# Kernel tuning notes

Measured on AMD Instinct MI355X. Metric: run time of the kernel, lower is better.

Reference implementation:

```python
import jax, jax.numpy as jnp
import numpy as np

N_NODES = 50000
N_EDGES = 800000
N_GRAPHS = 256
IN_CH = 128
HID = 256
FFN = 256
OUT = 1


def xavier(key, shape):
    fan_in, fan_out = shape[0], shape[1]
    a = jnp.sqrt(6.0 / (fan_in + fan_out))
    return jax.random.uniform(key, shape, jnp.float32, -a, a)


def setup_inputs() -> dict:
    key = jax.random.key(0)
    ks = jax.random.split(key, 12)
    x = jax.random.normal(ks[0], (N_NODES, IN_CH), jnp.float32)
    edge_index = jax.random.randint(ks[1], (2, N_EDGES), 0, N_NODES, jnp.int32)
    batch = jnp.sort(jax.random.randint(ks[2], (N_NODES,), 0, N_GRAPHS, jnp.int32))
    return {
        "x": x,
        "edge_index": edge_index,
        "batch": batch,
        # GCNConv layers (glorot weight, zero bias as in PyG reset_parameters)
        "W1": xavier(ks[3], (IN_CH, HID)), "b1": jnp.zeros((HID,), jnp.float32),
        "W2": xavier(ks[4], (HID, HID)),   "b2": jnp.zeros((HID,), jnp.float32),
        "W3": xavier(ks[5], (HID, HID)),   "b3": jnp.zeros((HID,), jnp.float32),
        # FFN: Linear(HID, FFN) then final Linear(FFN, OUT)
        "Wf": xavier(ks[6], (HID, FFN)),   "bf": jnp.zeros((FFN,), jnp.float32),
        "Wo": xavier(ks[7], (FFN, OUT)),   "bo": jnp.zeros((OUT,), jnp.float32),
    }


def _gcn_norm(edge_index, n_nodes):
    # add self-loops, compute symmetric normalization D^-1/2 (A+I) D^-1/2
    loops = jnp.arange(n_nodes, dtype=edge_index.dtype)
    row = jnp.concatenate([edge_index[0], loops])
    col = jnp.concatenate([edge_index[1], loops])
    deg = jax.ops.segment_sum(jnp.ones_like(col, jnp.float32), col, num_segments=n_nodes)
    dis = jnp.where(deg > 0, jax.lax.rsqrt(jnp.maximum(deg, 1.0)), 0.0)
    norm = dis[row] * dis[col]  # [E+N]
    return row, col, norm


def _gcn_conv(x, W, b, row, col, norm, n_nodes):
    xw = x @ W                                   # [N, H]
    msg = xw[row] * norm[:, None]                # gather + scale  [E+N, H]
    out = jax.ops.segment_sum(msg, col, num_segments=n_nodes)
    return out + b


def reference(x, edge_index, batch, W1, b1, W2, b2, W3, b3, Wf, bf, Wo, bo):
    row, col, norm = _gcn_norm(edge_index, N_NODES)
    h = jax.nn.relu(_gcn_conv(x, W1, b1, row, col, norm, N_NODES))
    h = jax.nn.relu(_gcn_conv(h, W2, b2, row, col, norm, N_NODES))
    h = jax.nn.relu(_gcn_conv(h, W3, b3, row, col, norm, N_NODES))
    # global mean pool over graphs
    counts = jax.ops.segment_sum(jnp.ones((N_NODES,), jnp.float32), batch, num_segments=N_GRAPHS)
    pooled = jax.ops.segment_sum(h, batch, num_segments=N_GRAPHS) / jnp.maximum(counts, 1.0)[:, None]
    # FFN (dropout is identity in eval mode): Linear -> ReLU -> final Linear
    g = jax.nn.relu(pooled @ Wf + bf)
    out = g @ Wo + bo
    return out
```

## Files before the change

### kernel.cpp

```cpp
#include <hip/hip_runtime.h>
#include <hip/hip_bf16.h>
#include <hip/hip_fp16.h>


#define THREADS 256

typedef _Float16 f16x8 __attribute__((ext_vector_type(8)));
typedef float    f32x4 __attribute__((ext_vector_type(4)));


__global__ void degree_goff_kernel(const int* __restrict__ col, int* __restrict__ deg, int E,
                                   const int* __restrict__ batch, int* __restrict__ goff,
                                   int N, int G) {
    int i = blockIdx.x * THREADS + threadIdx.x;
    if (i < E) atomicAdd(&deg[col[i]], 1);
    if (i < N) {
        int b1 = batch[i];
        int b0 = (i == 0) ? -1 : batch[i - 1];
        for (int g = b0 + 1; g <= b1; ++g) goff[g] = i;
        if (i == N - 1) {
            for (int g = b1 + 1; g <= G; ++g) goff[g] = N;
        }
    }
}

__global__ __launch_bounds__(256) void scanA_kernel(
    const int* __restrict__ in, int* __restrict__ out, int* __restrict__ bsum,
    float* __restrict__ dis, int n) {
    __shared__ int wsum[4];
    int i0 = blockIdx.x * 1024 + threadIdx.x * 4;
    int lane = threadIdx.x & 63, wid = threadIdx.x >> 6;
    int v0 = 0, v1 = 0, v2 = 0, v3 = 0;
    if (i0 + 3 < n) {
        int4 v = *(const int4*)&in[i0];
        v0 = v.x; v1 = v.y; v2 = v.z; v3 = v.w;
    } else {
        if (i0 + 0 < n) v0 = in[i0 + 0];
        if (i0 + 1 < n) v1 = in[i0 + 1];
        if (i0 + 2 < n) v2 = in[i0 + 2];
        if (i0 + 3 < n) v3 = in[i0 + 3];
    }
    if (i0 + 0 < n) dis[i0 + 0] = rsqrtf((float)(v0 + 1));
    if (i0 + 1 < n) dis[i0 + 1] = rsqrtf((float)(v1 + 1));
    if (i0 + 2 < n) dis[i0 + 2] = rsqrtf((float)(v2 + 1));
    if (i0 + 3 < n) dis[i0 + 3] = rsqrtf((float)(v3 + 1));
    int s = v0 + v1 + v2 + v3;
    int inc = s;
    #pragma unroll
    for (int d = 1; d < 64; d <<= 1) {
        int t = __shfl_up(inc, d);
        if (lane >= d) inc += t;
    }
    if (lane == 63) wsum[wid] = inc;
    __syncthreads();
    int add = 0;
    for (int w = 0; w < wid; ++w) add += wsum[w];
    int ex = add + inc - s;
    if (i0 + 0 < n) out[i0 + 0] = ex;
    if (i0 + 1 < n) out[i0 + 1] = ex + v0;
    if (i0 + 2 < n) out[i0 + 2] = ex + v0 + v1;
    if (i0 + 3 < n) out[i0 + 3] = ex + v0 + v1 + v2;
    if (threadIdx.x == 255) bsum[blockIdx.x] = add + inc;
}

__global__ void scanB_kernel(int* __restrict__ bsum, int* __restrict__ total_slot, int nb) {
    int lane = threadIdx.x;
    int v = (lane < nb) ? bsum[lane] : 0;
    int inc = v;
    #pragma unroll
    for (int d = 1; d < 64; d <<= 1) {
        int t = __shfl_up(inc, d);
        if (lane >= d) inc += t;
    }
    if (lane < nb) bsum[lane] = inc - v;
    if (lane == 63) *total_slot = inc;
}

__global__ void csr_fill_kernel(const int* __restrict__ row, const int* __restrict__ col,
                                const int* __restrict__ offs, int* __restrict__ deg,
                                int* __restrict__ srcs, int E) {
    int e = blockIdx.x * THREADS + threadIdx.x;
    if (e < E) {
        int c = col[e];
        int old = atomicSub(&deg[c], 1);
        srcs[offs[c] + old - 1] = row[e];
    }
}

__global__ void convert_kernel(
    int* __restrict__ offs, const int* __restrict__ bsum, int Nfix,
    const float* __restrict__ X, const float* __restrict__ dis,
    _Float16* __restrict__ Xs, int total8, int IC,
    const float* __restrict__ W1, _Float16* __restrict__ W1t, int k1,
    const float* __restrict__ W2, _Float16* __restrict__ W2t,
    const float* __restrict__ W3, _Float16* __restrict__ W3t) {
    int i = blockIdx.x * THREADS + threadIdx.x;
    if (i < Nfix) {
        offs[i] += bsum[i >> 10];
        return;
    }
    int j = i - Nfix;
    if (j < total8) {
        int idx = j * 8;
        float d = dis[idx / IC];
        float4 a = *(const float4*)&X[idx];
        float4 b = *(const float4*)&X[idx + 4];
        f16x8 o;
        o[0] = (_Float16)(d * a.x); o[1] = (_Float16)(d * a.y);
        o[2] = (_Float16)(d * a.z); o[3] = (_Float16)(d * a.w);
        o[4] = (_Float16)(d * b.x); o[5] = (_Float16)(d * b.y);
        o[6] = (_Float16)(d * b.z); o[7] = (_Float16)(d * b.w);
        *(f16x8*)&Xs[idx] = o;
        return;
    }
    j -= total8;
    int n1 = k1 * 256;
    if (j < n1) {
        int k = j >> 8, n = j & 255;
        W1t[n * k1 + k] = (_Float16)W1[j];
        return;
    }
    j -= n1;
    if (j < 65536) {
        int k = j >> 8, n = j & 255;
        W2t[n * 256 + k] = (_Float16)W2[j];
        return;
    }
    j -= 65536;
    if (j < 65536) {
        int k = j >> 8, n = j & 255;
        W3t[n * 256 + k] = (_Float16)W3[j];
    }
}


template<int LPN>
__global__ __launch_bounds__(256) void aggregate_f16_kernel(
    const _Float16* __restrict__ X, const int* __restrict__ offs,
    const int* __restrict__ srcs, const float* __restrict__ dis,
    _Float16* __restrict__ A, int N) {
    constexpr int NPB = 256 / LPN;
    int node = blockIdx.x * NPB + threadIdx.x / LPN;
    if (node >= N) return;
    int lane = threadIdx.x % LPN;
    const f16x8* Xv = (const f16x8*)X;
    f16x8 self = Xv[(size_t)node * LPN + lane];
    float acc[8], acc2[8];
    #pragma unroll
    for (int j = 0; j < 8; ++j) { acc[j] = (float)self[j]; acc2[j] = 0.f; }
    int s = offs[node], e = offs[node + 1];
    int i = s;
    for (; i + 4 <= e; i += 4) {
        int s0 = srcs[i], s1 = srcs[i + 1], s2 = srcs[i + 2], s3 = srcs[i + 3];
        f16x8 v0 = Xv[(size_t)s0 * LPN + lane];
        f16x8 v1 = Xv[(size_t)s1 * LPN + lane];
        f16x8 v2 = Xv[(size_t)s2 * LPN + lane];
        f16x8 v3 = Xv[(size_t)s3 * LPN + lane];
        #pragma unroll
        for (int j = 0; j < 8; ++j) {
            acc[j]  += (float)v0[j] + (float)v2[j];
            acc2[j] += (float)v1[j] + (float)v3[j];
        }
    }
    for (; i < e; ++i) {
        int s0 = srcs[i];
        f16x8 v0 = Xv[(size_t)s0 * LPN + lane];
        #pragma unroll
        for (int j = 0; j < 8; ++j) acc[j] += (float)v0[j];
    }
    float dn = dis[node];
    f16x8 o;
    #pragma unroll
    for (int j = 0; j < 8; ++j) o[j] = (_Float16)(dn * (acc[j] + acc2[j]));
    ((f16x8*)A)[(size_t)node * LPN + lane] = o;
}


template<int K, int MODE>
__global__ __launch_bounds__(256) void gemm_f16_kernel(
    const _Float16* __restrict__ A, const _Float16* __restrict__ B,
    const float* __restrict__ bias, const float* __restrict__ dscale,
    _Float16* __restrict__ H, float* __restrict__ pooled,
    const int* __restrict__ batch, int M) {
    constexpr int BM = 128, BN = 128, LST = 40;
    __shared__ _Float16 As[BM * LST];
    __shared__ _Float16 Bs[BN * LST];
    __shared__ int bsh[BM];
    int lin = blockIdx.x;
    int y = (lin >> 4) * 8 + (lin & 7);
    int xh = (lin >> 3) & 1;
    int MT = (M + 127) >> 7;
    if (y >= MT) return;
    int tid = threadIdx.x;
    int m0 = y * BM, n0 = xh * BN;
    int wid = tid >> 6, lane = tid & 63;
    int wm = (wid & 1) * 64, wn = (wid >> 1) * 64;
    int l16 = lane & 15, quad = lane >> 4;

    if (MODE == 2) {
        if (tid < BM) bsh[tid] = batch[min(m0 + tid, M - 1)];
    }

    f32x4 acc[4][4] = {};

    #pragma unroll
    for (int k0 = 0; k0 < K; k0 += 32) {
        #pragma unroll
        for (int rep = 0; rep < 2; ++rep) {
            int idx = tid + rep * 256;
            int r = idx >> 2, seg = idx & 3;
            int gr = m0 + r;
            uint4 va = make_uint4(0, 0, 0, 0);
            if (gr < M) va = *(const uint4*)&A[(size_t)gr * K + k0 + seg * 8];
            *(uint4*)&As[r * LST + seg * 8] = va;
            uint4 vb = *(const uint4*)&B[(size_t)(n0 + r) * K + k0 + seg * 8];
            *(uint4*)&Bs[r * LST + seg * 8] = vb;
        }
        __syncthreads();
        f16x8 bh[4];
        #pragma unroll
        for (int ni = 0; ni < 4; ++ni) {
            int n = wn + ni * 16 + l16;
            bh[ni] = *(const f16x8*)&Bs[n * LST + quad * 8];
        }
        #pragma unroll
        for (int mi = 0; mi < 4; ++mi) {
            int m = wm + mi * 16 + l16;
            f16x8 ah = *(const f16x8*)&As[m * LST + quad * 8];
            #pragma unroll
            for (int ni = 0; ni < 4; ++ni) {
                acc[mi][ni] = __builtin_amdgcn_mfma_f32_16x16x32_f16(ah, bh[ni], acc[mi][ni], 0, 0, 0);
            }
        }
        __syncthreads();
    }

    #pragma unroll
    for (int mi = 0; mi < 4; ++mi) {
        int base_local = wm + mi * 16;
        int g0 = 0, g15 = 0;
        if (MODE == 2) { g0 = bsh[base_local]; g15 = bsh[base_local + 15]; }
        #pragma unroll
        for (int ni = 0; ni < 4; ++ni) {
            int col = n0 + wn + ni * 16 + l16;
            float bv = bias[col];
            if (MODE == 1) {
                #pragma unroll
                for (int r = 0; r < 4; ++r) {
                    int grow = m0 + base_local + quad * 4 + r;
                    if (grow < M) {
                        float v = fmaxf(acc[mi][ni][r] + bv, 0.f) * dscale[grow];
                        H[(size_t)grow * 256 + col] = (_Float16)v;
                    }
                }
            } else {
                if (g0 == g15) {
                    float p = 0.f;
                    #pragma unroll
                    for (int r = 0; r < 4; ++r) {
                        int grow = m0 + base_local + quad * 4 + r;
                        float v = fmaxf(acc[mi][ni][r] + bv, 0.f);
                        p += (grow < M) ? v : 0.f;
                    }
                    p += __shfl_xor(p, 16);
                    p += __shfl_xor(p, 32);
                    if (quad == 0) atomicAdd(&pooled[g0 * 256 + col], p);
                } else {
                    #pragma unroll
                    for (int r = 0; r < 4; ++r) {
                        int local = base_local + quad * 4 + r;
                        int grow = m0 + local;
                        if (grow < M) {
                            float v = fmaxf(acc[mi][ni][r] + bv, 0.f);
                            atomicAdd(&pooled[bsh[local] * 256 + col], v);
                        }
                    }
                }
            }
        }
    }
}


__global__ __launch_bounds__(256) void ffn_kernel(
    const float* __restrict__ pooled, const int* __restrict__ goff,
    const float* __restrict__ Wf, const float* __restrict__ bf,
    const float* __restrict__ Wo, const float* __restrict__ bo,
    float* __restrict__ out) {
    __shared__ float p[256];
    __shared__ float red[256];
    int g = blockIdx.x, t = threadIdx.x;
    int cnt = goff[g + 1] - goff[g];
    float inv = 1.f / (float)max(cnt, 1);
    p[t] = pooled[g * 256 + t] * inv;
    __syncthreads();
    float s = bf[t];
    #pragma unroll 8
    for (int k = 0; k < 256; ++k) s = fmaf(p[k], Wf[k * 256 + t], s);
    float gv = fmaxf(s, 0.f);
    red[t] = gv * Wo[t];
    __syncthreads();
    for (int o = 128; o > 0; o >>= 1) {
        if (t < o) red[t] += red[t + o];
        __syncthreads();
    }
    if (t == 0) out[g] = red[0] + bo[0];
}


extern "C" void kernel_launch(void* const* d_in, const int* in_sizes, int n_in,
                              void* d_out, int out_size, void* d_ws, size_t ws_size,
                              hipStream_t stream) {
    const float* x   = (const float*)d_in[0];
    const int*   ei  = (const int*)d_in[1];
    const int*   bat = (const int*)d_in[2];
    const float* W1  = (const float*)d_in[3];
    const float* b1  = (const float*)d_in[4];
    const float* W2  = (const float*)d_in[5];
    const float* b2  = (const float*)d_in[6];
    const float* W3  = (const float*)d_in[7];
    const float* b3  = (const float*)d_in[8];
    const float* Wf  = (const float*)d_in[9];
    const float* bf  = (const float*)d_in[10];
    const float* Wo  = (const float*)d_in[11];
    const float* bo  = (const float*)d_in[12];
    float* out = (float*)d_out;

    const int N  = in_sizes[2];
    const int E  = in_sizes[1] / 2;
    const int IC = in_sizes[0] / N;
    const int HID = 256;
    const int G  = out_size;
    const int* row = ei;
    const int* col = ei + E;

    char* w = (char*)d_ws;
    size_t off = 0;
    auto alloc = [&](size_t bytes) -> void* {
        void* p = w + off;
        off += (bytes + 255) & ~(size_t)255;
        return p;
    };
    int*   deg    = (int*)alloc((size_t)N * 4);
    float* pooled = (float*)alloc((size_t)G * HID * 4);
    float* dis    = (float*)alloc((size_t)N * 4);
    int*   offs   = (int*)alloc((size_t)(N + 1) * 4);
    int*   srcs   = (int*)alloc((size_t)E * 4);
    int*   goff   = (int*)alloc((size_t)(G + 1) * 4);
    int*   bsum   = (int*)alloc((size_t)64 * 4);
    _Float16* W1t = (_Float16*)alloc((size_t)HID * IC * 2);
    _Float16* W2t = (_Float16*)alloc((size_t)HID * HID * 2);
    _Float16* W3t = (_Float16*)alloc((size_t)HID * HID * 2);
    _Float16* Xs  = (_Float16*)alloc((size_t)N * IC * 2);
    _Float16* Ah  = (_Float16*)alloc((size_t)N * HID * 2);
    _Float16* Hs  = (_Float16*)alloc((size_t)N * HID * 2);
    (void)ws_size; (void)n_in;

    size_t zlen = (((size_t)N * 4 + 255) & ~(size_t)255) + (size_t)G * HID * 4;
    hipMemsetAsync(deg, 0, zlen, stream);

    int nb = (N + 1023) / 1024;
    degree_goff_kernel<<<(E + THREADS - 1) / THREADS, THREADS, 0, stream>>>(
        col, deg, E, bat, goff, N, G);
    scanA_kernel<<<nb, 256, 0, stream>>>(deg, offs, bsum, dis, N);
    scanB_kernel<<<1, 64, 0, stream>>>(bsum, &offs[N], nb);

    int total8 = N * IC / 8;
    int conv_total = N + total8 + IC * HID + HID * HID + HID * HID;
    convert_kernel<<<(conv_total + THREADS - 1) / THREADS, THREADS, 0, stream>>>(
        offs, bsum, N, x, dis, Xs, total8, IC, W1, W1t, IC, W2, W2t, W3, W3t);

    csr_fill_kernel<<<(E + THREADS - 1) / THREADS, THREADS, 0, stream>>>(row, col, offs, deg, srcs, E);

    int MT = (N + 127) / 128;
    int gblocks = 2 * (((MT + 7) / 8) * 8);
    aggregate_f16_kernel<16><<<(N + 15) / 16, 256, 0, stream>>>(Xs, offs, srcs, dis, Ah, N);
    gemm_f16_kernel<128, 1><<<gblocks, 256, 0, stream>>>(Ah, W1t, b1, dis, Hs, nullptr, nullptr, N);
    aggregate_f16_kernel<32><<<(N + 7) / 8, 256, 0, stream>>>(Hs, offs, srcs, dis, Ah, N);
    gemm_f16_kernel<256, 1><<<gblocks, 256, 0, stream>>>(Ah, W2t, b2, dis, Hs, nullptr, nullptr, N);
    aggregate_f16_kernel<32><<<(N + 7) / 8, 256, 0, stream>>>(Hs, offs, srcs, dis, Ah, N);
    gemm_f16_kernel<256, 2><<<gblocks, 256, 0, stream>>>(Ah, W3t, b3, nullptr, nullptr, pooled, bat, N);

    ffn_kernel<<<G, 256, 0, stream>>>(pooled, goff, Wf, bf, Wo, bo, out);
}
```

Baseline: 439.2 us.

## Make GEMM persistent with full weight matrix resident in shared memory

Replaces the tiled 128x128 GEMM with a persistent kernel. Each block loads the whole transposed weight matrix into LDS once, then loops over 64-row tiles. A fragments are read straight from global memory into registers and the per-k-step syncthreads are gone. This removes repeated weight staging and barrier overhead, but needs large LDS (about 132KB for K=256), which limits occupancy to one block per CU and puts heavy register pressure on holding all A fragments.

```diff
diff --git a/kernel.cpp b/kernel.cpp
--- a/kernel.cpp
+++ b/kernel.cpp
@@ -177,102 +177,92 @@
 
 
 template<int K, int MODE>
-__global__ __launch_bounds__(256) void gemm_f16_kernel(
-    const _Float16* __restrict__ A, const _Float16* __restrict__ B,
+__global__ __launch_bounds__(256) void gemm_ws_kernel(
+    const _Float16* __restrict__ A, const _Float16* __restrict__ Bt,
     const float* __restrict__ bias, const float* __restrict__ dscale,
     _Float16* __restrict__ H, float* __restrict__ pooled,
-    const int* __restrict__ batch, int M) {
-    constexpr int BM = 128, BN = 128, LST = 40;
-    __shared__ _Float16 As[BM * LST];
-    __shared__ _Float16 Bs[BN * LST];
-    __shared__ int bsh[BM];
-    int lin = blockIdx.x;
-    int y = (lin >> 4) * 8 + (lin & 7);
-    int xh = (lin >> 3) & 1;
-    int MT = (M + 127) >> 7;
-    if (y >= MT) return;
+    const int* __restrict__ batch, int M, int tiles) {
+    extern __shared__ _Float16 Bs[];
+    constexpr int LSB = K + 8;
+    constexpr int KC = K / 32;
     int tid = threadIdx.x;
-    int m0 = y * BM, n0 = xh * BN;
+
+    constexpr int CHUNKS = 256 * K / 8;
+    for (int idx = tid; idx < CHUNKS; idx += 256) {
+        int r = idx / (K / 8), seg = idx % (K / 8);
+        *(uint4*)&Bs[r * LSB + seg * 8] = *(const uint4*)&Bt[(size_t)r * K + seg * 8];
+    }
+    __syncthreads();
+
     int wid = tid >> 6, lane = tid & 63;
-    int wm = (wid & 1) * 64, wn = (wid >> 1) * 64;
     int l16 = lane & 15, quad = lane >> 4;
-
-    if (MODE == 2) {
-        if (tid < BM) bsh[tid] = batch[min(m0 + tid, M - 1)];
-    }
-
-    f32x4 acc[4][4] = {};
-
-    #pragma unroll
-    for (int k0 = 0; k0 < K; k0 += 32) {
-        #pragma unroll
-        for (int rep = 0; rep < 2; ++rep) {
-            int idx = tid + rep * 256;
-            int r = idx >> 2, seg = idx & 3;
-            int gr = m0 + r;
-            uint4 va = make_uint4(0, 0, 0, 0);
-            if (gr < M) va = *(const uint4*)&A[(size_t)gr * K + k0 + seg * 8];
-            *(uint4*)&As[r * LST + seg * 8] = va;
-            uint4 vb = *(const uint4*)&B[(size_t)(n0 + r) * K + k0 + seg * 8];
-            *(uint4*)&Bs[r * LST + seg * 8] = vb;
-        }
-        __syncthreads();
-        f16x8 bh[4];
-        #pragma unroll
-        for (int ni = 0; ni < 4; ++ni) {
-            int n = wn + ni * 16 + l16;
-            bh[ni] = *(const f16x8*)&Bs[n * LST + quad * 8];
-        }
+    int wn = wid * 64;
+
+    for (int tile = blockIdx.x; tile < tiles; tile += gridDim.x) {
+        int m0 = tile * 64;
+        f32x4 acc[4][4] = {};
+        f16x8 ahp[4][KC];
         #pragma unroll
         for (int mi = 0; mi < 4; ++mi) {
-            int m = wm + mi * 16 + l16;
-            f16x8 ah = *(const f16x8*)&As[m * LST + quad * 8];
+            size_t ar = (size_t)min(m0 + mi * 16 + l16, M - 1) * K + quad * 8;
+            #pragma unroll
+            for (int kc = 0; kc < KC; ++kc)
+                ahp[mi][kc] = *(const f16x8*)&A[ar + kc * 32];
+        }
+        #pragma unroll
+        for (int kc = 0; kc < KC; ++kc) {
+            f16x8 bh[4];
+            #pragma unroll
+            for (int ni = 0; ni < 4; ++ni)
+                bh[ni] = *(const f16x8*)&Bs[(wn + ni * 16 + l16) * LSB + kc * 32 + quad * 8];
+            #pragma unroll
+            for (int mi = 0; mi < 4; ++mi) {
+                #pragma unroll
+                for (int ni = 0; ni < 4; ++ni)
+                    acc[mi][ni] = __builtin_amdgcn_mfma_f32_16x16x32_f16(ahp[mi][kc], bh[ni], acc[mi][ni], 0, 0, 0);
+            }
+        }
+        #pragma unroll
+        for (int mi = 0; mi < 4; ++mi) {
+            int rbase = m0 + mi * 16;
+            int g0 = 0, g15 = 0;
+            if (MODE == 2) {
+                g0  = batch[min(rbase, M - 1)];
+                g15 = batch[min(rbase + 15, M - 1)];
+            }
             #pragma unroll
             for (int ni = 0; ni < 4; ++ni) {
-                acc[mi][ni] = __builtin_amdgcn_mfma_f32_16x16x32_f16(ah, bh[ni], acc[mi][ni], 0, 0, 0);
-            }
-        }
-        __syncthreads();
-    }
-
-    #pragma unroll
-    for (int mi = 0; mi < 4; ++mi) {
-        int base_local = wm + mi * 16;
-        int g0 = 0, g15 = 0;
-        if (MODE == 2) { g0 = bsh[base_local]; g15 = bsh[base_local + 15]; }
-        #pragma unroll
-        for (int ni = 0; ni < 4; ++ni) {
-            int col = n0 + wn + ni * 16 + l16;
-            float bv = bias[col];
-            if (MODE == 1) {
-                #pragma unroll
-                for (int r = 0; r < 4; ++r) {
-                    int grow = m0 + base_local + quad * 4 + r;
-                    if (grow < M) {
-                        float v = fmaxf(acc[mi][ni][r] + bv, 0.f) * dscale[grow];
-                        H[(size_t)grow * 256 + col] = (_Float16)v;
-                    }
-                }
-            } else {
-                if (g0 == g15) {
-                    float p = 0.f;
+                int col = wn + ni * 16 + l16;
+                float bv = bias[col];
+                if (MODE == 1) {
                     #pragma unroll
                     for (int r = 0; r < 4; ++r) {
-                        int grow = m0 + base_local + quad * 4 + r;
-                        float v = fmaxf(acc[mi][ni][r] + bv, 0.f);
-                        p += (grow < M) ? v : 0.f;
+                        int grow = rbase + quad * 4 + r;
+                        if (grow < M) {
+                            float v = fmaxf(acc[mi][ni][r] + bv, 0.f) * dscale[grow];
+                            H[(size_t)grow * 256 + col] = (_Float16)v;
+                        }
                     }
-                    p += __shfl_xor(p, 16);
-                    p += __shfl_xor(p, 32);
-                    if (quad == 0) atomicAdd(&pooled[g0 * 256 + col], p);
                 } else {
-                    #pragma unroll
-                    for (int r = 0; r < 4; ++r) {
-                        int local = base_local + quad * 4 + r;
-                        int grow = m0 + local;
-                        if (grow < M) {
+                    if (g0 == g15) {
+                        float p = 0.f;
+                        #pragma unroll
+                        for (int r = 0; r < 4; ++r) {
+                            int grow = rbase + quad * 4 + r;
                             float v = fmaxf(acc[mi][ni][r] + bv, 0.f);
-                            atomicAdd(&pooled[bsh[local] * 256 + col], v);
+                            p += (grow < M) ? v : 0.f;
+                        }
+                        p += __shfl_xor(p, 16);
+                        p += __shfl_xor(p, 32);
+                        if (quad == 0) atomicAdd(&pooled[g0 * 256 + col], p);
+                    } else {
+                        #pragma unroll
+                        for (int r = 0; r < 4; ++r) {
+                            int grow = rbase + quad * 4 + r;
+                            if (grow < M) {
+                                float v = fmaxf(acc[mi][ni][r] + bv, 0.f);
+                                atomicAdd(&pooled[batch[grow] * 256 + col], v);
+                            }
                         }
                     }
                 }
@@ -356,6 +346,15 @@
     _Float16* Hs  = (_Float16*)alloc((size_t)N * HID * 2);
     (void)ws_size; (void)n_in;
 
+    size_t lds128 = (size_t)256 * (128 + 8) * 2;
+    size_t lds256 = (size_t)256 * (256 + 8) * 2;
+    (void)hipFuncSetAttribute((const void*)gemm_ws_kernel<128, 1>,
+                              hipFuncAttributeMaxDynamicSharedMemorySize, (int)lds128);
+    (void)hipFuncSetAttribute((const void*)gemm_ws_kernel<256, 1>,
+                              hipFuncAttributeMaxDynamicSharedMemorySize, (int)lds256);
+    (void)hipFuncSetAttribute((const void*)gemm_ws_kernel<256, 2>,
+                              hipFuncAttributeMaxDynamicSharedMemorySize, (int)lds256);
+
     size_t zlen = (((size_t)N * 4 + 255) & ~(size_t)255) + (size_t)G * HID * 4;
     hipMemsetAsync(deg, 0, zlen, stream);
 
@@ -372,14 +371,13 @@
 
     csr_fill_kernel<<<(E + THREADS - 1) / THREADS, THREADS, 0, stream>>>(row, col, offs, deg, srcs, E);
 
-    int MT = (N + 127) / 128;
-    int gblocks = 2 * (((MT + 7) / 8) * 8);
+    int tiles = (N + 63) / 64;
     aggregate_f16_kernel<16><<<(N + 15) / 16, 256, 0, stream>>>(Xs, offs, srcs, dis, Ah, N);
-    gemm_f16_kernel<128, 1><<<gblocks, 256, 0, stream>>>(Ah, W1t, b1, dis, Hs, nullptr, nullptr, N);
+    gemm_ws_kernel<128, 1><<<512, 256, lds128, stream>>>(Ah, W1t, b1, dis, Hs, nullptr, nullptr, N, tiles);
     aggregate_f16_kernel<32><<<(N + 7) / 8, 256, 0, stream>>>(Hs, offs, srcs, dis, Ah, N);
-    gemm_f16_kernel<256, 1><<<gblocks, 256, 0, stream>>>(Ah, W2t, b2, dis, Hs, nullptr, nullptr, N);
+    gemm_ws_kernel<256, 1><<<256, 256, lds256, stream>>>(Ah, W2t, b2, dis, Hs, nullptr, nullptr, N, tiles);
     aggregate_f16_kernel<32><<<(N + 7) / 8, 256, 0, stream>>>(Hs, offs, srcs, dis, Ah, N);
-    gemm_f16_kernel<256, 2><<<gblocks, 256, 0, stream>>>(Ah, W3t, b3, nullptr, nullptr, pooled, bat, N);
+    gemm_ws_kernel<256, 2><<<256, 256, lds256, stream>>>(Ah, W3t, b3, nullptr, nullptr, pooled, bat, N, tiles);
 
     ffn_kernel<<<G, 256, 0, stream>>>(pooled, goff, Wf, bf, Wo, bo, out);
 }
```

After: 503.3 us. 1.15x slower.
